# Kernel optimization log

Measured on AMD Instinct MI355X. Metric: run time of the kernel, lower is better.

Reference implementation:

```python
import jax, jax.numpy as jnp
import numpy as np

TEMPERATURE = 0.1
THR = 0.2
BORDER_RM = 2


def setup_inputs() -> dict:
    key = jax.random.key(0)
    k0, k1 = jax.random.split(key)
    N, L, S, C = 2, 4800, 4800, 256
    return {
        "feat_c0": jax.random.normal(k0, (N, L, C), dtype=jnp.float32),
        "feat_c1": jax.random.normal(k1, (N, S, C), dtype=jnp.float32),
        "h0c": 60, "w0c": 80, "h1c": 60, "w1c": 80,
    }


def _border_valid(h, w, bd):
    # Faithful to torch mask_border: only the FIRST `bd` rows/cols are masked
    # (the negative slices m[:, -bd:0] in the source are empty no-ops).
    vh = jnp.arange(h) >= bd
    vw = jnp.arange(w) >= bd
    return (vh[:, None] & vw[None, :]).reshape(-1)  # [h*w]


def reference(feat_c0, feat_c1, h0c, w0c, h1c, w1c):
    C = feat_c0.shape[-1]
    scale = 1.0 / (C ** 0.5)  # 'sqrt_feat_dim' feature normalizer
    f0 = feat_c0 * scale
    f1 = feat_c1 * scale

    # dual-softmax confidence matrix [N, L, S]
    sim = jnp.einsum("nlc,nsc->nls", f0, f1) / TEMPERATURE
    conf = jax.nn.softmax(sim, axis=1) * jax.nn.softmax(sim, axis=2)

    # threshold + border removal (no padding masks in data)
    mask = conf > THR
    valid0 = _border_valid(h0c, w0c, BORDER_RM)  # [L]
    valid1 = _border_valid(h1c, w1c, BORDER_RM)  # [S]
    mask = mask & valid0[None, :, None] & valid1[None, None, :]

    # mutual nearest neighbour filtering
    mask = mask & (conf == conf.max(axis=2, keepdims=True)) \
                & (conf == conf.max(axis=1, keepdims=True))

    # match extraction (JIT-friendly padded form):
    # j_ids[b, i] = column of the (unique) True in row i; match_mask marks valid rows.
    j_ids = jnp.argmax(mask, axis=2)               # [N, L] int
    match_mask = jnp.any(mask, axis=2)             # [N, L] bool
    mconf = jnp.take_along_axis(conf, j_ids[..., None], axis=2)[..., 0]
    mconf = jnp.where(match_mask, mconf, 0.0)      # [N, L]

    return conf, match_mask, j_ids, mconf
```

## Files before the change

### kernel.cpp

```cpp
#include <hip/hip_runtime.h>


#define Ncst 2
#define Lc 4800
#define Sc 4800
#define Cc 256
#define K2 512
#define LP 4864
#define THRC 0.2f

typedef float f32x4 __attribute__((ext_vector_type(4)));
typedef _Float16 f16x8 __attribute__((ext_vector_type(8)));

#define AS1(p) ((__attribute__((address_space(1))) void*)(p))
#define AS3(p) ((__attribute__((address_space(3))) void*)(p))

__global__ __launch_bounds__(256) void init_kernel(float* __restrict__ rs, float* __restrict__ cs)
{
    int i = blockIdx.x * 256 + threadIdx.x;
    if (i < Ncst * Lc) { rs[i] = 0.f; cs[i] = 0.f; }
}

__global__ __launch_bounds__(256) void convert_kernel(
    const float* __restrict__ f0, const float* __restrict__ f1,
    unsigned short* __restrict__ A2, unsigned short* __restrict__ B2)
{
    int idx = blockIdx.x * 256 + threadIdx.x;
    if (idx >= Ncst * LP * (Cc / 8)) return;
    int k8  = idx & (Cc / 8 - 1);
    int row = (idx >> 5) % LP;
    int n   = idx / (LP * (Cc / 8));
    size_t base = ((size_t)n * LP + row) * K2 + k8 * 8;

    float av[8], bv[8];
    if (row < Lc) {
        const float4* pa = (const float4*)(f0 + ((size_t)n * Lc + row) * Cc + k8 * 8);
        float4 a0 = pa[0], a1 = pa[1];
        av[0]=a0.x; av[1]=a0.y; av[2]=a0.z; av[3]=a0.w;
        av[4]=a1.x; av[5]=a1.y; av[6]=a1.z; av[7]=a1.w;
        const float4* pb = (const float4*)(f1 + ((size_t)n * Sc + row) * Cc + k8 * 8);
        float4 b0 = pb[0], b1 = pb[1];
        bv[0]=b0.x; bv[1]=b0.y; bv[2]=b0.z; bv[3]=b0.w;
        bv[4]=b1.x; bv[5]=b1.y; bv[6]=b1.z; bv[7]=b1.w;
    } else {
        for (int i = 0; i < 8; ++i) { av[i] = 0.f; bv[i] = 0.f; }
    }

    _Float16 ahi[8], alo[8], bhi[8];
#pragma unroll
    for (int i = 0; i < 8; ++i) {
        _Float16 h = (_Float16)av[i];
        ahi[i] = h;
        alo[i] = (_Float16)(av[i] - (float)h);
        bhi[i] = (_Float16)bv[i];
    }
    *(uint4*)&A2[base]       = *(uint4*)ahi;
    *(uint4*)&A2[base + 256] = *(uint4*)alo;
    *(uint4*)&B2[base]       = *(uint4*)bhi;
    *(uint4*)&B2[base + 256] = *(uint4*)bhi;
}

__global__ __launch_bounds__(256) void gemm_kernel(
    const unsigned short* __restrict__ A2, const unsigned short* __restrict__ B2,
    float* __restrict__ eout, float* __restrict__ rs, float* __restrict__ cs)
{
    __shared__ unsigned short lA[128 * 64];
    __shared__ unsigned short lB[128 * 64];

    int flat = blockIdx.x + 38 * blockIdx.y + 1444 * blockIdx.z;
    int m    = (flat & 7) * 361 + (flat >> 3);
    const int tn = m % 38;
    const int tm = (m / 38) % 38;
    const int n  = m / 1444;

    const int tid  = threadIdx.x;
    const int wave = tid >> 6;
    const int lane = tid & 63;
    const int wm   = wave >> 1;
    const int wn   = wave & 1;
    const int ml   = lane & 15;
    const int kq   = lane >> 4;

    const unsigned short* Ab = A2 + ((size_t)n * LP + (size_t)tm * 128) * K2;
    const unsigned short* Bb = B2 + ((size_t)n * LP + (size_t)tn * 128) * K2;

    f32x4 acc[4][4] = {};

    for (int k0 = 0; k0 < K2; k0 += 64) {
        __syncthreads();
#pragma unroll
        for (int cc = 0; cc < 4; ++cc) {
            int slot = (wave * 4 + cc) * 64 + lane;
            int row  = slot >> 3;
            int q    = (slot & 7) ^ (row & 7);
            const unsigned short* ga = Ab + (size_t)row * K2 + (k0 + q * 8);
            const unsigned short* gb = Bb + (size_t)row * K2 + (k0 + q * 8);
            __builtin_amdgcn_global_load_lds(AS1(ga), AS3(lA + (size_t)slot * 8), 16, 0, 0);
            __builtin_amdgcn_global_load_lds(AS1(gb), AS3(lB + (size_t)slot * 8), 16, 0, 0);
        }
        __syncthreads();

#pragma unroll
        for (int s = 0; s < 2; ++s) {
            f16x8 af[4], bfr[4];
#pragma unroll
            for (int i = 0; i < 4; ++i) {
                int arow = wm * 64 + i * 16 + ml;
                int aq   = (s * 4 + kq) ^ (arow & 7);
                af[i] = *(const f16x8*)&lA[((size_t)arow * 8 + aq) * 8];
                int brow = wn * 64 + i * 16 + ml;
                int bq   = (s * 4 + kq) ^ (brow & 7);
                bfr[i] = *(const f16x8*)&lB[((size_t)brow * 8 + bq) * 8];
            }
#pragma unroll
            for (int i = 0; i < 4; ++i)
#pragma unroll
                for (int j = 0; j < 4; ++j)
                    acc[i][j] = __builtin_amdgcn_mfma_f32_16x16x32_f16(af[i], bfr[j], acc[i][j], 0, 0, 0);
        }
    }

    const float alpha = 5.0f / 128.0f;
#pragma unroll
    for (int i = 0; i < 4; ++i) {
#pragma unroll
        for (int r = 0; r < 4; ++r) {
            int gl = tm * 128 + wm * 64 + i * 16 + kq * 4 + r;
            bool rok = gl < Lc;
#pragma unroll
            for (int j = 0; j < 4; ++j) {
                int gs = tn * 128 + wn * 64 + j * 16 + ml;
                bool ok = rok && (gs < Sc);
                float ev = ok ? __expf(acc[i][j][r] * alpha) : 0.f;
                acc[i][j][r] = ev;
                if (ok) eout[((size_t)n * Lc + gl) * Sc + gs] = ev;
            }
        }
    }
#pragma unroll
    for (int i = 0; i < 4; ++i) {
#pragma unroll
        for (int r = 0; r < 4; ++r) {
            float rp = acc[i][0][r] + acc[i][1][r] + acc[i][2][r] + acc[i][3][r];
            rp += __shfl_xor(rp, 1);
            rp += __shfl_xor(rp, 2);
            rp += __shfl_xor(rp, 4);
            rp += __shfl_xor(rp, 8);
            int gl = tm * 128 + wm * 64 + i * 16 + kq * 4 + r;
            if (ml == 0 && gl < Lc) atomicAdd(&rs[(size_t)n * Lc + gl], rp);
        }
    }
#pragma unroll
    for (int j = 0; j < 4; ++j) {
        float cp = 0.f;
#pragma unroll
        for (int i = 0; i < 4; ++i)
#pragma unroll
            for (int r = 0; r < 4; ++r) cp += acc[i][j][r];
        cp += __shfl_xor(cp, 16);
        cp += __shfl_xor(cp, 32);
        int gs = tn * 128 + wn * 64 + j * 16 + ml;
        if (kq == 0 && gs < Sc) atomicAdd(&cs[(size_t)n * Sc + gs], cp);
    }
}

__global__ __launch_bounds__(256) void inv_kernel(
    const float* __restrict__ rs, const float* __restrict__ cs,
    float* __restrict__ rsinv, float* __restrict__ csinv)
{
    int i = blockIdx.x * 256 + threadIdx.x;
    if (i < Ncst * Lc) { rsinv[i] = 1.0f / rs[i]; csinv[i] = 1.0f / cs[i]; }
}

__global__ __launch_bounds__(256) void conf_kernel(
    float* __restrict__ confio,
    const float* __restrict__ rsinv, const float* __restrict__ csinv,
    float* __restrict__ rcm)
{
    __shared__ float sw[4];
    int b = blockIdx.x;
    int n = b / Lc;
    f32x4* row = (f32x4*)(confio + (size_t)b * Sc);
    const f32x4* civ = (const f32x4*)(csinv + (size_t)n * Sc);
    int tid = threadIdx.x;
    float riv = rsinv[b];
    float lmax = 0.f;
    for (int v = tid; v < Sc / 4; v += 256) {
        f32x4 e4 = row[v];
        f32x4 c4 = civ[v];
        f32x4 o  = e4 * e4 * riv * c4;
        row[v] = o;
        lmax = fmaxf(lmax, fmaxf(fmaxf(o.x, o.y), fmaxf(o.z, o.w)));
    }
#pragma unroll
    for (int off = 1; off < 64; off <<= 1) lmax = fmaxf(lmax, __shfl_xor(lmax, off));
    if ((tid & 63) == 0) sw[tid >> 6] = lmax;
    __syncthreads();
    if (tid == 0) rcm[b] = fmaxf(fmaxf(sw[0], sw[1]), fmaxf(sw[2], sw[3]));
}

__global__ __launch_bounds__(256) void finalize_kernel(
    const float* __restrict__ conf, const float* __restrict__ rcm,
    const int* __restrict__ h0p, const int* __restrict__ w0p,
    const int* __restrict__ h1p, const int* __restrict__ w1p,
    float* __restrict__ out_match, float* __restrict__ out_j, float* __restrict__ out_mconf)
{
    int i = blockIdx.x * 256 + threadIdx.x;
    if (i >= Ncst * Lc) return;
    int n = i / Lc, l = i % Lc;
    float mm = rcm[i];
    float fm = 0.f, fj = 0.f, fc = 0.f;
    if (mm > THRC) {
        int w0 = *w0p, w1 = *w1p;
        if ((l / w0) >= 2 && (l % w0) >= 2) {
            const float* rowp = conf + ((size_t)n * Lc + l) * Sc;
            for (int s = 0; s < Sc; ++s) {
                float c = rowp[s];
                if (c == mm && (s / w1) >= 2 && (s % w1) >= 2) {
                    bool ismax = true;
                    const float* colp = conf + (size_t)n * Lc * Sc + s;
                    for (int lp = 0; lp < Lc; ++lp) {
                        if (colp[(size_t)lp * Sc] > c) { ismax = false; break; }
                    }
                    if (ismax) { fm = 1.f; fj = (float)s; fc = c; break; }
                }
            }
        }
    }
    out_match[i] = fm; out_j[i] = fj; out_mconf[i] = fc;
}

extern "C" void kernel_launch(void* const* d_in, const int* in_sizes, int n_in,
                              void* d_out, int out_size, void* d_ws, size_t ws_size,
                              hipStream_t stream) {
    const float* f0 = (const float*)d_in[0];
    const float* f1 = (const float*)d_in[1];
    const int* h0p = (const int*)d_in[2];
    const int* w0p = (const int*)d_in[3];
    const int* h1p = (const int*)d_in[4];
    const int* w1p = (const int*)d_in[5];

    char* ws = (char*)d_ws;
    unsigned short* A2 = (unsigned short*)ws;
    unsigned short* B2 = (unsigned short*)(ws + 9961472);
    float* rs    = (float*)(ws + 19922944);
    float* cs    = (float*)(ws + 19961344);
    float* rsinv = (float*)(ws + 19999744);
    float* csinv = (float*)(ws + 20038144);
    float* rcm   = (float*)(ws + 20076544);

    float* conf      = (float*)d_out;
    float* out_match = conf + (size_t)Ncst * Lc * Sc;
    float* out_j     = out_match + Ncst * Lc;
    float* out_mconf = out_j + Ncst * Lc;

    init_kernel<<<(Ncst * Lc + 255) / 256, 256, 0, stream>>>(rs, cs);

    convert_kernel<<<(Ncst * LP * (Cc / 8) + 255) / 256, 256, 0, stream>>>(f0, f1, A2, B2);

    dim3 gg(LP / 128, LP / 128, Ncst);
    gemm_kernel<<<gg, 256, 0, stream>>>(A2, B2, conf, rs, cs);

    inv_kernel<<<(Ncst * Lc + 255) / 256, 256, 0, stream>>>(rs, cs, rsinv, csinv);

    conf_kernel<<<Ncst * Lc, 256, 0, stream>>>(conf, rsinv, csinv, rcm);

    finalize_kernel<<<(Ncst * Lc + 255) / 256, 256, 0, stream>>>(
        conf, rcm, h0p, w0p, h1p, w1p, out_match, out_j, out_mconf);
}
```

Before: 337.8 us.

## Recompute GEMM in second pass to fuse softmax normalization and row max

Replaces the write-exp, inv, and conf-rescale kernels with two GEMM passes. The first pass only accumulates row and column exp sums. The second recomputes the GEMM and writes the final conf directly, with the row max taken by an atomicMax on the float bits. This removes a full read-modify-write of the 184MB conf matrix at the cost of doing the GEMM twice. The K loop is also reworked into a double-buffered pipeline with 32-wide K tiles and a different swizzle.

Measured after the change: 405.6 us. 20.1% more time.

```diff
diff --git a/kernel.cpp b/kernel.cpp
--- a/kernel.cpp
+++ b/kernel.cpp
@@ -15,10 +15,11 @@
 #define AS1(p) ((__attribute__((address_space(1))) void*)(p))
 #define AS3(p) ((__attribute__((address_space(3))) void*)(p))
 
-__global__ __launch_bounds__(256) void init_kernel(float* __restrict__ rs, float* __restrict__ cs)
+__global__ __launch_bounds__(256) void init_kernel(
+    float* __restrict__ rs, float* __restrict__ cs, float* __restrict__ rcm)
 {
     int i = blockIdx.x * 256 + threadIdx.x;
-    if (i < Ncst * Lc) { rs[i] = 0.f; cs[i] = 0.f; }
+    if (i < Ncst * Lc) { rs[i] = 0.f; cs[i] = 0.f; rcm[i] = 0.f; }
 }
 
 __global__ __launch_bounds__(256) void convert_kernel(
@@ -60,12 +61,14 @@
     *(uint4*)&B2[base + 256] = *(uint4*)bhi;
 }
 
+template <int PASS>
 __global__ __launch_bounds__(256) void gemm_kernel(
     const unsigned short* __restrict__ A2, const unsigned short* __restrict__ B2,
-    float* __restrict__ eout, float* __restrict__ rs, float* __restrict__ cs)
-{
-    __shared__ unsigned short lA[128 * 64];
-    __shared__ unsigned short lB[128 * 64];
+    float* __restrict__ out, float* __restrict__ rs, float* __restrict__ cs,
+    int* __restrict__ rcm)
+{
+    __shared__ unsigned short lA[2][128 * 32];
+    __shared__ unsigned short lB[2][128 * 32];
 
     int flat = blockIdx.x + 38 * blockIdx.y + 1444 * blockIdx.z;
     int m    = (flat & 7) * 361 + (flat >> 3);
@@ -84,119 +87,132 @@
     const unsigned short* Ab = A2 + ((size_t)n * LP + (size_t)tm * 128) * K2;
     const unsigned short* Bb = B2 + ((size_t)n * LP + (size_t)tn * 128) * K2;
 
+    const int s0 = (wave * 2 + 0) * 64 + lane;
+    const int s1 = (wave * 2 + 1) * 64 + lane;
+    const int r0_ = s0 >> 2, q0 = (s0 & 3) ^ ((r0_ >> 1) & 3);
+    const int r1_ = s1 >> 2, q1 = (s1 & 3) ^ ((r1_ >> 1) & 3);
+    const unsigned short* gA0 = Ab + (size_t)r0_ * K2 + q0 * 8;
+    const unsigned short* gA1 = Ab + (size_t)r1_ * K2 + q1 * 8;
+    const unsigned short* gB0 = Bb + (size_t)r0_ * K2 + q0 * 8;
+    const unsigned short* gB1 = Bb + (size_t)r1_ * K2 + q1 * 8;
+
+    int aoff[4], boff[4];
+#pragma unroll
+    for (int i = 0; i < 4; ++i) {
+        int arow = wm * 64 + i * 16 + ml;
+        aoff[i] = (arow * 4 + (kq ^ ((arow >> 1) & 3))) * 8;
+        int brow = wn * 64 + i * 16 + ml;
+        boff[i] = (brow * 4 + (kq ^ ((brow >> 1) & 3))) * 8;
+    }
+
     f32x4 acc[4][4] = {};
 
-    for (int k0 = 0; k0 < K2; k0 += 64) {
+    __builtin_amdgcn_global_load_lds(AS1(gA0), AS3(&lA[0][s0 * 8]), 16, 0, 0);
+    __builtin_amdgcn_global_load_lds(AS1(gA1), AS3(&lA[0][s1 * 8]), 16, 0, 0);
+    __builtin_amdgcn_global_load_lds(AS1(gB0), AS3(&lB[0][s0 * 8]), 16, 0, 0);
+    __builtin_amdgcn_global_load_lds(AS1(gB1), AS3(&lB[0][s1 * 8]), 16, 0, 0);
+    __syncthreads();
+
+#pragma unroll
+    for (int t = 0; t < 16; ++t) {
+        const int buf = t & 1;
+        if (t < 15) {
+            const int ko = (t + 1) * 32;
+            __builtin_amdgcn_global_load_lds(AS1(gA0 + ko), AS3(&lA[buf ^ 1][s0 * 8]), 16, 0, 0);
+            __builtin_amdgcn_global_load_lds(AS1(gA1 + ko), AS3(&lA[buf ^ 1][s1 * 8]), 16, 0, 0);
+            __builtin_amdgcn_global_load_lds(AS1(gB0 + ko), AS3(&lB[buf ^ 1][s0 * 8]), 16, 0, 0);
+            __builtin_amdgcn_global_load_lds(AS1(gB1 + ko), AS3(&lB[buf ^ 1][s1 * 8]), 16, 0, 0);
+        }
+        f16x8 af[4], bfr[4];
+#pragma unroll
+        for (int i = 0; i < 4; ++i) {
+            af[i]  = *(const f16x8*)&lA[buf][aoff[i]];
+            bfr[i] = *(const f16x8*)&lB[buf][boff[i]];
+        }
+#pragma unroll
+        for (int i = 0; i < 4; ++i)
+#pragma unroll
+            for (int j = 0; j < 4; ++j)
+                acc[i][j] = __builtin_amdgcn_mfma_f32_16x16x32_f16(af[i], bfr[j], acc[i][j], 0, 0, 0);
         __syncthreads();
-#pragma unroll
-        for (int cc = 0; cc < 4; ++cc) {
-            int slot = (wave * 4 + cc) * 64 + lane;
-            int row  = slot >> 3;
-            int q    = (slot & 7) ^ (row & 7);
-            const unsigned short* ga = Ab + (size_t)row * K2 + (k0 + q * 8);
-            const unsigned short* gb = Bb + (size_t)row * K2 + (k0 + q * 8);
-            __builtin_amdgcn_global_load_lds(AS1(ga), AS3(lA + (size_t)slot * 8), 16, 0, 0);
-            __builtin_amdgcn_global_load_lds(AS1(gb), AS3(lB + (size_t)slot * 8), 16, 0, 0);
-        }
-        __syncthreads();
-
-#pragma unroll
-        for (int s = 0; s < 2; ++s) {
-            f16x8 af[4], bfr[4];
-#pragma unroll
-            for (int i = 0; i < 4; ++i) {
-                int arow = wm * 64 + i * 16 + ml;
-                int aq   = (s * 4 + kq) ^ (arow & 7);
-                af[i] = *(const f16x8*)&lA[((size_t)arow * 8 + aq) * 8];
-                int brow = wn * 64 + i * 16 + ml;
-                int bq   = (s * 4 + kq) ^ (brow & 7);
-                bfr[i] = *(const f16x8*)&lB[((size_t)brow * 8 + bq) * 8];
-            }
+    }
+
+    const float alpha = 5.0f / 128.0f;
+
+    if constexpr (PASS == 0) {
+#pragma unroll
+        for (int i = 0; i < 4; ++i) {
+#pragma unroll
+            for (int r = 0; r < 4; ++r) {
+                int gl = tm * 128 + wm * 64 + i * 16 + kq * 4 + r;
+                bool rok = gl < Lc;
+#pragma unroll
+                for (int j = 0; j < 4; ++j) {
+                    int gs = tn * 128 + wn * 64 + j * 16 + ml;
+                    bool ok = rok && (gs < Sc);
+                    acc[i][j][r] = ok ? __expf(acc[i][j][r] * alpha) : 0.f;
+                }
+            }
+        }
+#pragma unroll
+        for (int i = 0; i < 4; ++i) {
+#pragma unroll
+            for (int r = 0; r < 4; ++r) {
+                float rp = acc[i][0][r] + acc[i][1][r] + acc[i][2][r] + acc[i][3][r];
+                rp += __shfl_xor(rp, 1);
+                rp += __shfl_xor(rp, 2);
+                rp += __shfl_xor(rp, 4);
+                rp += __shfl_xor(rp, 8);
+                int gl = tm * 128 + wm * 64 + i * 16 + kq * 4 + r;
+                if (ml == 0 && gl < Lc) atomicAdd(&rs[(size_t)n * Lc + gl], rp);
+            }
+        }
+#pragma unroll
+        for (int j = 0; j < 4; ++j) {
+            float cp = 0.f;
 #pragma unroll
             for (int i = 0; i < 4; ++i)
 #pragma unroll
-                for (int j = 0; j < 4; ++j)
-                    acc[i][j] = __builtin_amdgcn_mfma_f32_16x16x32_f16(af[i], bfr[j], acc[i][j], 0, 0, 0);
-        }
-    }
-
-    const float alpha = 5.0f / 128.0f;
-#pragma unroll
-    for (int i = 0; i < 4; ++i) {
-#pragma unroll
-        for (int r = 0; r < 4; ++r) {
-            int gl = tm * 128 + wm * 64 + i * 16 + kq * 4 + r;
-            bool rok = gl < Lc;
-#pragma unroll
-            for (int j = 0; j < 4; ++j) {
-                int gs = tn * 128 + wn * 64 + j * 16 + ml;
-                bool ok = rok && (gs < Sc);
-                float ev = ok ? __expf(acc[i][j][r] * alpha) : 0.f;
-                acc[i][j][r] = ev;
-                if (ok) eout[((size_t)n * Lc + gl) * Sc + gs] = ev;
-            }
-        }
-    }
-#pragma unroll
-    for (int i = 0; i < 4; ++i) {
-#pragma unroll
-        for (int r = 0; r < 4; ++r) {
-            float rp = acc[i][0][r] + acc[i][1][r] + acc[i][2][r] + acc[i][3][r];
-            rp += __shfl_xor(rp, 1);
-            rp += __shfl_xor(rp, 2);
-            rp += __shfl_xor(rp, 4);
-            rp += __shfl_xor(rp, 8);
-            int gl = tm * 128 + wm * 64 + i * 16 + kq * 4 + r;
-            if (ml == 0 && gl < Lc) atomicAdd(&rs[(size_t)n * Lc + gl], rp);
-        }
-    }
-#pragma unroll
-    for (int j = 0; j < 4; ++j) {
-        float cp = 0.f;
-#pragma unroll
-        for (int i = 0; i < 4; ++i)
-#pragma unroll
-            for (int r = 0; r < 4; ++r) cp += acc[i][j][r];
-        cp += __shfl_xor(cp, 16);
-        cp += __shfl_xor(cp, 32);
-        int gs = tn * 128 + wn * 64 + j * 16 + ml;
-        if (kq == 0 && gs < Sc) atomicAdd(&cs[(size_t)n * Sc + gs], cp);
-    }
-}
-
-__global__ __launch_bounds__(256) void inv_kernel(
-    const float* __restrict__ rs, const float* __restrict__ cs,
-    float* __restrict__ rsinv, float* __restrict__ csinv)
-{
-    int i = blockIdx.x * 256 + threadIdx.x;
-    if (i < Ncst * Lc) { rsinv[i] = 1.0f / rs[i]; csinv[i] = 1.0f / cs[i]; }
-}
-
-__global__ __launch_bounds__(256) void conf_kernel(
-    float* __restrict__ confio,
-    const float* __restrict__ rsinv, const float* __restrict__ csinv,
-    float* __restrict__ rcm)
-{
-    __shared__ float sw[4];
-    int b = blockIdx.x;
-    int n = b / Lc;
-    f32x4* row = (f32x4*)(confio + (size_t)b * Sc);
-    const f32x4* civ = (const f32x4*)(csinv + (size_t)n * Sc);
-    int tid = threadIdx.x;
-    float riv = rsinv[b];
-    float lmax = 0.f;
-    for (int v = tid; v < Sc / 4; v += 256) {
-        f32x4 e4 = row[v];
-        f32x4 c4 = civ[v];
-        f32x4 o  = e4 * e4 * riv * c4;
-        row[v] = o;
-        lmax = fmaxf(lmax, fmaxf(fmaxf(o.x, o.y), fmaxf(o.z, o.w)));
-    }
-#pragma unroll
-    for (int off = 1; off < 64; off <<= 1) lmax = fmaxf(lmax, __shfl_xor(lmax, off));
-    if ((tid & 63) == 0) sw[tid >> 6] = lmax;
-    __syncthreads();
-    if (tid == 0) rcm[b] = fmaxf(fmaxf(sw[0], sw[1]), fmaxf(sw[2], sw[3]));
+                for (int r = 0; r < 4; ++r) cp += acc[i][j][r];
+            cp += __shfl_xor(cp, 16);
+            cp += __shfl_xor(cp, 32);
+            int gs = tn * 128 + wn * 64 + j * 16 + ml;
+            if (kq == 0 && gs < Sc) atomicAdd(&cs[(size_t)n * Sc + gs], cp);
+        }
+    } else {
+        float cin[4];
+#pragma unroll
+        for (int j = 0; j < 4; ++j) {
+            int gs = tn * 128 + wn * 64 + j * 16 + ml;
+            cin[j] = (gs < Sc) ? 1.0f / cs[(size_t)n * Sc + gs] : 0.f;
+        }
+#pragma unroll
+        for (int i = 0; i < 4; ++i) {
+#pragma unroll
+            for (int r = 0; r < 4; ++r) {
+                int gl = tm * 128 + wm * 64 + i * 16 + kq * 4 + r;
+                bool rok = gl < Lc;
+                float ri = rok ? 1.0f / rs[(size_t)n * Lc + gl] : 0.f;
+                float rmax = 0.f;
+#pragma unroll
+                for (int j = 0; j < 4; ++j) {
+                    int gs = tn * 128 + wn * 64 + j * 16 + ml;
+                    bool ok = rok && (gs < Sc);
+                    float ev = __expf(acc[i][j][r] * alpha);
+                    float c  = ev * ev * ri * cin[j];
+                    if (!ok) c = 0.f;
+                    if (ok) out[((size_t)n * Lc + gl) * Sc + gs] = c;
+                    rmax = fmaxf(rmax, c);
+                }
+                rmax = fmaxf(rmax, __shfl_xor(rmax, 1));
+                rmax = fmaxf(rmax, __shfl_xor(rmax, 2));
+                rmax = fmaxf(rmax, __shfl_xor(rmax, 4));
+                rmax = fmaxf(rmax, __shfl_xor(rmax, 8));
+                if (ml == 0 && rok)
+                    atomicMax(&rcm[(size_t)n * Lc + gl], __float_as_int(rmax));
+            }
+        }
+    }
 }
 
 __global__ __launch_bounds__(256) void finalize_kernel(
@@ -243,27 +259,22 @@
     char* ws = (char*)d_ws;
     unsigned short* A2 = (unsigned short*)ws;
     unsigned short* B2 = (unsigned short*)(ws + 9961472);
-    float* rs    = (float*)(ws + 19922944);
-    float* cs    = (float*)(ws + 19961344);
-    float* rsinv = (float*)(ws + 19999744);
-    float* csinv = (float*)(ws + 20038144);
-    float* rcm   = (float*)(ws + 20076544);
+    float* rs  = (float*)(ws + 19922944);
+    float* cs  = (float*)(ws + 19961344);
+    float* rcm = (float*)(ws + 19999744);
 
     float* conf      = (float*)d_out;
     float* out_match = conf + (size_t)Ncst * Lc * Sc;
     float* out_j     = out_match + Ncst * Lc;
     float* out_mconf = out_j + Ncst * Lc;
 
-    init_kernel<<<(Ncst * Lc + 255) / 256, 256, 0, stream>>>(rs, cs);
+    init_kernel<<<(Ncst * Lc + 255) / 256, 256, 0, stream>>>(rs, cs, rcm);
 
     convert_kernel<<<(Ncst * LP * (Cc / 8) + 255) / 256, 256, 0, stream>>>(f0, f1, A2, B2);
 
     dim3 gg(LP / 128, LP / 128, Ncst);
-    gemm_kernel<<<gg, 256, 0, stream>>>(A2, B2, conf, rs, cs);
-
-    inv_kernel<<<(Ncst * Lc + 255) / 256, 256, 0, stream>>>(rs, cs, rsinv, csinv);
-
-    conf_kernel<<<Ncst * Lc, 256, 0, stream>>>(conf, rsinv, csinv, rcm);
+    gemm_kernel<0><<<gg, 256, 0, stream>>>(A2, B2, nullptr, rs, cs, nullptr);
+    gemm_kernel<1><<<gg, 256, 0, stream>>>(A2, B2, conf, rs, cs, (int*)rcm);
 
     finalize_kernel<<<(Ncst * Lc + 255) / 256, 256, 0, stream>>>(
         conf, rcm, h0p, w0p, h1p, w1p, out_match, out_j, out_mconf);
```

## Use 256x256 double-buffered GEMM tiles with 8 waves and fold init into convert

Applied to the files above, without the earlier changes.

The GEMM moves from 128x128 tiles with 4 waves and a single LDS buffer to 256x256 tiles with 8 waves, double-buffered LDS, staged prefetch of the next K-slice interleaved with MFMA phases, explicit vmcnt waits, barriers and setprio. The XCD-aware block remapping is adjusted for the new grid. The zeroing of the row and column sums is folded into the convert kernel, which drops one launch. The goal is more data reuse per tile and hiding global-to-LDS latency, at the cost of more padded work (4864 rounds up to 19x256) and higher register pressure.

Measured after the change: 338.9 us. No clear change (+0.3%).

```diff
diff --git a/kernel.cpp b/kernel.cpp
--- a/kernel.cpp
+++ b/kernel.cpp
@@ -15,17 +15,13 @@
 #define AS1(p) ((__attribute__((address_space(1))) void*)(p))
 #define AS3(p) ((__attribute__((address_space(3))) void*)(p))
 
-__global__ __launch_bounds__(256) void init_kernel(float* __restrict__ rs, float* __restrict__ cs)
-{
-    int i = blockIdx.x * 256 + threadIdx.x;
-    if (i < Ncst * Lc) { rs[i] = 0.f; cs[i] = 0.f; }
-}
-
 __global__ __launch_bounds__(256) void convert_kernel(
     const float* __restrict__ f0, const float* __restrict__ f1,
-    unsigned short* __restrict__ A2, unsigned short* __restrict__ B2)
+    unsigned short* __restrict__ A2, unsigned short* __restrict__ B2,
+    float* __restrict__ rs, float* __restrict__ cs)
 {
     int idx = blockIdx.x * 256 + threadIdx.x;
+    if (idx < Ncst * Lc) { rs[idx] = 0.f; cs[idx] = 0.f; }
     if (idx >= Ncst * LP * (Cc / 8)) return;
     int k8  = idx & (Cc / 8 - 1);
     int row = (idx >> 5) % LP;
@@ -60,93 +56,125 @@
     *(uint4*)&B2[base + 256] = *(uint4*)bhi;
 }
 
-__global__ __launch_bounds__(256) void gemm_kernel(
+__global__ __launch_bounds__(512, 2) void gemm_kernel(
     const unsigned short* __restrict__ A2, const unsigned short* __restrict__ B2,
     float* __restrict__ eout, float* __restrict__ rs, float* __restrict__ cs)
 {
-    __shared__ unsigned short lA[128 * 64];
-    __shared__ unsigned short lB[128 * 64];
-
-    int flat = blockIdx.x + 38 * blockIdx.y + 1444 * blockIdx.z;
-    int m    = (flat & 7) * 361 + (flat >> 3);
-    const int tn = m % 38;
-    const int tm = (m / 38) % 38;
-    const int n  = m / 1444;
+    __shared__ __attribute__((aligned(16))) unsigned short lds[2][2][2][8192];
+
+    int flat = blockIdx.x + 19 * blockIdx.y + 361 * blockIdx.z;
+    int xcd = flat & 7, o8 = flat >> 3;
+    const int qc = 722 / 8, rc = 722 % 8;
+    int wg = (xcd < rc ? xcd * (qc + 1) : rc * (qc + 1) + (xcd - rc) * qc) + o8;
+    const int tn = wg % 19;
+    const int tm = (wg / 19) % 19;
+    const int n  = wg / 361;
 
     const int tid  = threadIdx.x;
     const int wave = tid >> 6;
     const int lane = tid & 63;
-    const int wm   = wave >> 1;
-    const int wn   = wave & 1;
+    const int wm   = wave >> 2;
+    const int wn   = wave & 3;
     const int ml   = lane & 15;
     const int kq   = lane >> 4;
 
-    const unsigned short* Ab = A2 + ((size_t)n * LP + (size_t)tm * 128) * K2;
-    const unsigned short* Bb = B2 + ((size_t)n * LP + (size_t)tn * 128) * K2;
-
-    f32x4 acc[4][4] = {};
-
-    for (int k0 = 0; k0 < K2; k0 += 64) {
-        __syncthreads();
-#pragma unroll
-        for (int cc = 0; cc < 4; ++cc) {
-            int slot = (wave * 4 + cc) * 64 + lane;
-            int row  = slot >> 3;
-            int q    = (slot & 7) ^ (row & 7);
-            const unsigned short* ga = Ab + (size_t)row * K2 + (k0 + q * 8);
-            const unsigned short* gb = Bb + (size_t)row * K2 + (k0 + q * 8);
-            __builtin_amdgcn_global_load_lds(AS1(ga), AS3(lA + (size_t)slot * 8), 16, 0, 0);
-            __builtin_amdgcn_global_load_lds(AS1(gb), AS3(lB + (size_t)slot * 8), 16, 0, 0);
+    const unsigned short* Ab = A2 + ((size_t)n * LP + (size_t)tm * 256) * K2;
+    const unsigned short* Bb = B2 + ((size_t)n * LP + (size_t)tn * 256) * K2;
+
+    const unsigned short *pA[2][2], *pB[2][2];
+    int sidx_[2];
+#pragma unroll
+    for (int c = 0; c < 2; ++c) {
+        int s = c * 512 + tid;
+        sidx_[c] = s;
+        int row = s >> 2;
+        int q   = (s & 3) ^ ((row >> 1) & 3);
+#pragma unroll
+        for (int kh = 0; kh < 2; ++kh) {
+            pA[kh][c] = Ab + (size_t)row * K2 + kh * 32 + q * 8;
+            pB[kh][c] = Bb + (size_t)row * K2 + kh * 32 + q * 8;
         }
-        __syncthreads();
-
-#pragma unroll
-        for (int s = 0; s < 2; ++s) {
-            f16x8 af[4], bfr[4];
-#pragma unroll
-            for (int i = 0; i < 4; ++i) {
-                int arow = wm * 64 + i * 16 + ml;
-                int aq   = (s * 4 + kq) ^ (arow & 7);
-                af[i] = *(const f16x8*)&lA[((size_t)arow * 8 + aq) * 8];
-                int brow = wn * 64 + i * 16 + ml;
-                int bq   = (s * 4 + kq) ^ (brow & 7);
-                bfr[i] = *(const f16x8*)&lB[((size_t)brow * 8 + bq) * 8];
-            }
-#pragma unroll
-            for (int i = 0; i < 4; ++i)
-#pragma unroll
-                for (int j = 0; j < 4; ++j)
-                    acc[i][j] = __builtin_amdgcn_mfma_f32_16x16x32_f16(af[i], bfr[j], acc[i][j], 0, 0, 0);
-        }
+    }
+
+#define STAGE_A(bb, kh, tt) do { \
+    __builtin_amdgcn_global_load_lds(AS1(pA[kh][0] + (tt) * 64), AS3(&lds[bb][0][kh][sidx_[0] * 8]), 16, 0, 0); \
+    __builtin_amdgcn_global_load_lds(AS1(pA[kh][1] + (tt) * 64), AS3(&lds[bb][0][kh][sidx_[1] * 8]), 16, 0, 0); \
+    } while (0)
+#define STAGE_B(bb, kh, tt) do { \
+    __builtin_amdgcn_global_load_lds(AS1(pB[kh][0] + (tt) * 64), AS3(&lds[bb][1][kh][sidx_[0] * 8]), 16, 0, 0); \
+    __builtin_amdgcn_global_load_lds(AS1(pB[kh][1] + (tt) * 64), AS3(&lds[bb][1][kh][sidx_[1] * 8]), 16, 0, 0); \
+    } while (0)
+#define READA(bb, m_, ks) do { _Pragma("unroll") for (int i_ = 0; i_ < 4; ++i_) { \
+    int r_ = wm * 128 + (m_) * 64 + i_ * 16 + ml; \
+    af[i_] = *(const f16x8*)&lds[bb][0][ks][(r_ * 4 + (kq ^ ((r_ >> 1) & 3))) * 8]; } } while (0)
+#define READB(bb, ks) do { _Pragma("unroll") for (int j_ = 0; j_ < 4; ++j_) { \
+    int r_ = wn * 64 + j_ * 16 + ml; \
+    bf_[j_] = *(const f16x8*)&lds[bb][1][ks][(r_ * 4 + (kq ^ ((r_ >> 1) & 3))) * 8]; } } while (0)
+#define MFMAQ(m_) do { _Pragma("unroll") for (int i_ = 0; i_ < 4; ++i_) _Pragma("unroll") for (int j_ = 0; j_ < 4; ++j_) \
+    acc[(m_) * 4 + i_][j_] = __builtin_amdgcn_mfma_f32_16x16x32_f16(af[i_], bf_[j_], acc[(m_) * 4 + i_][j_], 0, 0, 0); } while (0)
+
+    f32x4 acc[8][4] = {};
+
+    STAGE_A(0, 0, 0); STAGE_B(0, 0, 0); STAGE_A(0, 1, 0); STAGE_B(0, 1, 0);
+    asm volatile("s_waitcnt vmcnt(4)" ::: "memory");
+    __builtin_amdgcn_s_barrier();
+
+#pragma unroll
+    for (int t = 0; t < 8; ++t) {
+        const int b  = t & 1;
+        const int nb = b ^ 1;
+        const bool pf = (t < 7);
+        f16x8 af[4], bf_[4];
+        READB(b, 0); READA(b, 0, 0);
+        if (pf) STAGE_A(nb, 0, t + 1);
+        __builtin_amdgcn_s_barrier();
+        __builtin_amdgcn_s_setprio(1); MFMAQ(0); __builtin_amdgcn_s_setprio(0);
+        __builtin_amdgcn_s_barrier();
+        READA(b, 1, 0);
+        if (pf) { STAGE_B(nb, 0, t + 1); asm volatile("s_waitcnt vmcnt(4)" ::: "memory"); }
+        else    { asm volatile("s_waitcnt vmcnt(0)" ::: "memory"); }
+        __builtin_amdgcn_s_barrier();
+        __builtin_amdgcn_s_setprio(1); MFMAQ(1); __builtin_amdgcn_s_setprio(0);
+        __builtin_amdgcn_s_barrier();
+        READB(b, 1); READA(b, 0, 1);
+        if (pf) STAGE_A(nb, 1, t + 1);
+        __builtin_amdgcn_s_barrier();
+        __builtin_amdgcn_s_setprio(1); MFMAQ(0); __builtin_amdgcn_s_setprio(0);
+        __builtin_amdgcn_s_barrier();
+        READA(b, 1, 1);
+        if (pf) { STAGE_B(nb, 1, t + 1); asm volatile("s_waitcnt vmcnt(4)" ::: "memory"); }
+        __builtin_amdgcn_s_barrier();
+        __builtin_amdgcn_s_setprio(1); MFMAQ(1); __builtin_amdgcn_s_setprio(0);
+        __builtin_amdgcn_s_barrier();
     }
 
     const float alpha = 5.0f / 128.0f;
 #pragma unroll
-    for (int i = 0; i < 4; ++i) {
+    for (int ii = 0; ii < 8; ++ii) {
 #pragma unroll
         for (int r = 0; r < 4; ++r) {
-            int gl = tm * 128 + wm * 64 + i * 16 + kq * 4 + r;
+            int gl = tm * 256 + wm * 128 + ii * 16 + kq * 4 + r;
             bool rok = gl < Lc;
 #pragma unroll
             for (int j = 0; j < 4; ++j) {
-                int gs = tn * 128 + wn * 64 + j * 16 + ml;
+                int gs = tn * 256 + wn * 64 + j * 16 + ml;
                 bool ok = rok && (gs < Sc);
-                float ev = ok ? __expf(acc[i][j][r] * alpha) : 0.f;
-                acc[i][j][r] = ev;
+                float ev = ok ? __expf(acc[ii][j][r] * alpha) : 0.f;
+                acc[ii][j][r] = ev;
                 if (ok) eout[((size_t)n * Lc + gl) * Sc + gs] = ev;
             }
         }
     }
 #pragma unroll
-    for (int i = 0; i < 4; ++i) {
+    for (int ii = 0; ii < 8; ++ii) {
 #pragma unroll
         for (int r = 0; r < 4; ++r) {
-            float rp = acc[i][0][r] + acc[i][1][r] + acc[i][2][r] + acc[i][3][r];
+            float rp = acc[ii][0][r] + acc[ii][1][r] + acc[ii][2][r] + acc[ii][3][r];
             rp += __shfl_xor(rp, 1);
             rp += __shfl_xor(rp, 2);
             rp += __shfl_xor(rp, 4);
             rp += __shfl_xor(rp, 8);
-            int gl = tm * 128 + wm * 64 + i * 16 + kq * 4 + r;
+            int gl = tm * 256 + wm * 128 + ii * 16 + kq * 4 + r;
             if (ml == 0 && gl < Lc) atomicAdd(&rs[(size_t)n * Lc + gl], rp);
         }
     }
@@ -154,14 +182,19 @@
     for (int j = 0; j < 4; ++j) {
         float cp = 0.f;
 #pragma unroll
-        for (int i = 0; i < 4; ++i)
-#pragma unroll
-            for (int r = 0; r < 4; ++r) cp += acc[i][j][r];
+        for (int ii = 0; ii < 8; ++ii)
+#pragma unroll
+            for (int r = 0; r < 4; ++r) cp += acc[ii][j][r];
         cp += __shfl_xor(cp, 16);
         cp += __shfl_xor(cp, 32);
-        int gs = tn * 128 + wn * 64 + j * 16 + ml;
+        int gs = tn * 256 + wn * 64 + j * 16 + ml;
         if (kq == 0 && gs < Sc) atomicAdd(&cs[(size_t)n * Sc + gs], cp);
     }
+#undef STAGE_A
+#undef STAGE_B
+#undef READA
+#undef READB
+#undef MFMAQ
 }
 
 __global__ __launch_bounds__(256) void inv_kernel(
@@ -254,12 +287,10 @@
     float* out_j     = out_match + Ncst * Lc;
     float* out_mconf = out_j + Ncst * Lc;
 
-    init_kernel<<<(Ncst * Lc + 255) / 256, 256, 0, stream>>>(rs, cs);
-
-    convert_kernel<<<(Ncst * LP * (Cc / 8) + 255) / 256, 256, 0, stream>>>(f0, f1, A2, B2);
-
-    dim3 gg(LP / 128, LP / 128, Ncst);
-    gemm_kernel<<<gg, 256, 0, stream>>>(A2, B2, conf, rs, cs);
+    convert_kernel<<<(Ncst * LP * (Cc / 8) + 255) / 256, 256, 0, stream>>>(f0, f1, A2, B2, rs, cs);
+
+    dim3 gg(19, 19, Ncst);
+    gemm_kernel<<<gg, 512, 0, stream>>>(A2, B2, conf, rs, cs);
 
     inv_kernel<<<(Ncst * Lc + 255) / 256, 256, 0, stream>>>(rs, cs, rsinv, csinv);
 
```
